# Optimization experiments

Measured on AMD Instinct MI355X. Metric: run time of the kernel, lower is better.

## Reference

```python
import jax, jax.numpy as jnp
import numpy as np


def setup_inputs() -> dict:
    key = jax.random.key(0)
    k1, k2 = jax.random.split(key)
    B, K = 128, 1024
    coordinates = jax.random.normal(k1, (B, K, 3), dtype=jnp.float32)
    precision_squared = jax.random.uniform(k2, (1,), dtype=jnp.float32)
    return {"coordinates": coordinates, "precision_squared": precision_squared}


def reference(coordinates, precision_squared):
    norms = jnp.sum(coordinates * coordinates, axis=-1)  # [B, K]
    gram = jnp.einsum('bkd,bjd->bkj', coordinates, coordinates)  # [B, K, K]
    distances = norms[:, :, None] - 2.0 * gram + norms[:, None, :]  # [B, K, K]
    A = jnp.exp(-distances * precision_squared[0])
    A = jax.nn.softmax(A, axis=-1)  # row softmax (axis=1 of the per-sample [K,K])
    return A
```

## Files before the change

kernel.cpp:

```cpp
#include <hip/hip_runtime.h>


#define K_PTS 1024
#define ROWS_PER_BLOCK 4

__global__ __launch_bounds__(256) void adj_softmax_kernel(
    const float* __restrict__ coords,
    const float* __restrict__ prec,
    float* __restrict__ out,
    int B) {
  __shared__ float sx[K_PTS];
  __shared__ float sy[K_PTS];
  __shared__ float sz[K_PTS];

  const int tid  = threadIdx.x;
  const int lane = tid & 63;
  const int wave = tid >> 6;
  const int tilesPerBatch = K_PTS / ROWS_PER_BLOCK;
  const int b    = blockIdx.x / tilesPerBatch;
  const int tile = blockIdx.x % tilesPerBatch;

  const float p = prec[0];

  {
    const float* cb = coords + (size_t)b * (K_PTS * 3);
    const int p0 = tid * 4;
    const float4* src = (const float4*)(cb + (size_t)p0 * 3);
    float4 a0 = src[0];
    float4 a1 = src[1];
    float4 a2 = src[2];
    sx[p0 + 0] = a0.x; sy[p0 + 0] = a0.y; sz[p0 + 0] = a0.z;
    sx[p0 + 1] = a0.w; sy[p0 + 1] = a1.x; sz[p0 + 1] = a1.y;
    sx[p0 + 2] = a1.z; sy[p0 + 2] = a1.w; sz[p0 + 2] = a2.x;
    sx[p0 + 3] = a2.y; sy[p0 + 3] = a2.z; sz[p0 + 3] = a2.w;
  }
  __syncthreads();

  const int i = tile * ROWS_PER_BLOCK + wave;
  const float xi = sx[i];
  const float yi = sy[i];
  const float zi = sz[i];

  float4 e[4];
  float acc = 0.0f;

#pragma unroll
  for (int t = 0; t < 4; ++t) {
    const int j0 = 4 * lane + 256 * t;
    float4 vx = *(const float4*)&sx[j0];
    float4 vy = *(const float4*)&sy[j0];
    float4 vz = *(const float4*)&sz[j0];

    float dx, dy, dz, d, xv;
    float4 ev;

    dx = vx.x - xi; dy = vy.x - yi; dz = vz.x - zi;
    d  = fmaf(dx, dx, fmaf(dy, dy, dz * dz));
    xv = __expf(-p * d);
    ev.x = __expf(xv - 1.0f);

    dx = vx.y - xi; dy = vy.y - yi; dz = vz.y - zi;
    d  = fmaf(dx, dx, fmaf(dy, dy, dz * dz));
    xv = __expf(-p * d);
    ev.y = __expf(xv - 1.0f);

    dx = vx.z - xi; dy = vy.z - yi; dz = vz.z - zi;
    d  = fmaf(dx, dx, fmaf(dy, dy, dz * dz));
    xv = __expf(-p * d);
    ev.z = __expf(xv - 1.0f);

    dx = vx.w - xi; dy = vy.w - yi; dz = vz.w - zi;
    d  = fmaf(dx, dx, fmaf(dy, dy, dz * dz));
    xv = __expf(-p * d);
    ev.w = __expf(xv - 1.0f);

    e[t] = ev;
    acc += (ev.x + ev.y) + (ev.z + ev.w);
  }

#pragma unroll
  for (int off = 32; off > 0; off >>= 1) {
    acc += __shfl_xor(acc, off, 64);
  }
  const float inv = 1.0f / acc;

  float* orow = out + ((size_t)b * K_PTS + i) * K_PTS;
#pragma unroll
  for (int t = 0; t < 4; ++t) {
    float4 ev = e[t];
    ev.x *= inv; ev.y *= inv; ev.z *= inv; ev.w *= inv;
    *(float4*)&orow[4 * lane + 256 * t] = ev;
  }
}

extern "C" void kernel_launch(void* const* d_in, const int* in_sizes, int n_in,
                              void* d_out, int out_size, void* d_ws, size_t ws_size,
                              hipStream_t stream) {
  const float* coords = (const float*)d_in[0];
  const float* prec   = (const float*)d_in[1];
  float* out = (float*)d_out;

  const int B = in_sizes[0] / (K_PTS * 3);
  const int grid = B * (K_PTS / ROWS_PER_BLOCK);

  adj_softmax_kernel<<<grid, 256, 0, stream>>>(coords, prec, out, B);
}
```

Baseline: 512.3 us.

## Process multiple row tiles per block and use nontemporal output stores

Each block now stages a batch's coordinates into shared memory once and loops over 64 rows instead of 4. Column coordinates are kept in registers across rows, which cuts redundant global loads, LDS staging and block launch overhead. Output stores become nontemporal to avoid cache pollution on the large write stream. Fewer blocks reduce parallel slack and raise register pressure.

```diff
diff --git a/kernel.cpp b/kernel.cpp
--- a/kernel.cpp
+++ b/kernel.cpp
@@ -2,9 +2,13 @@
 
 
 #define K_PTS 1024
-#define ROWS_PER_BLOCK 4
+#define THREADS 256
+#define TILES_PER_BLOCK 16
+#define BLOCKS_PER_BATCH 16
 
-__global__ __launch_bounds__(256) void adj_softmax_kernel(
+typedef float vf4 __attribute__((ext_vector_type(4)));
+
+__global__ __launch_bounds__(THREADS, 4) void adj_softmax_kernel(
     const float* __restrict__ coords,
     const float* __restrict__ prec,
     float* __restrict__ out,
@@ -13,14 +17,14 @@
   __shared__ float sy[K_PTS];
   __shared__ float sz[K_PTS];
 
-  const int tid  = threadIdx.x;
-  const int lane = tid & 63;
-  const int wave = tid >> 6;
-  const int tilesPerBatch = K_PTS / ROWS_PER_BLOCK;
-  const int b    = blockIdx.x / tilesPerBatch;
-  const int tile = blockIdx.x % tilesPerBatch;
+  const int tid   = threadIdx.x;
+  const int lane  = tid & 63;
+  const int wave  = tid >> 6;
+  const int b     = blockIdx.x / BLOCKS_PER_BATCH;
+  const int chunk = blockIdx.x % BLOCKS_PER_BATCH;
 
-  const float p = prec[0];
+  const float p  = prec[0];
+  const float np = -p;
 
   {
     const float* cb = coords + (size_t)b * (K_PTS * 3);
@@ -36,60 +40,67 @@
   }
   __syncthreads();
 
-  const int i = tile * ROWS_PER_BLOCK + wave;
-  const float xi = sx[i];
-  const float yi = sy[i];
-  const float zi = sz[i];
-
-  float4 e[4];
-  float acc = 0.0f;
-
+  float4 vx[4], vy[4], vz[4];
 #pragma unroll
   for (int t = 0; t < 4; ++t) {
     const int j0 = 4 * lane + 256 * t;
-    float4 vx = *(const float4*)&sx[j0];
-    float4 vy = *(const float4*)&sy[j0];
-    float4 vz = *(const float4*)&sz[j0];
-
-    float dx, dy, dz, d, xv;
-    float4 ev;
-
-    dx = vx.x - xi; dy = vy.x - yi; dz = vz.x - zi;
-    d  = fmaf(dx, dx, fmaf(dy, dy, dz * dz));
-    xv = __expf(-p * d);
-    ev.x = __expf(xv - 1.0f);
-
-    dx = vx.y - xi; dy = vy.y - yi; dz = vz.y - zi;
-    d  = fmaf(dx, dx, fmaf(dy, dy, dz * dz));
-    xv = __expf(-p * d);
-    ev.y = __expf(xv - 1.0f);
-
-    dx = vx.z - xi; dy = vy.z - yi; dz = vz.z - zi;
-    d  = fmaf(dx, dx, fmaf(dy, dy, dz * dz));
-    xv = __expf(-p * d);
-    ev.z = __expf(xv - 1.0f);
-
-    dx = vx.w - xi; dy = vy.w - yi; dz = vz.w - zi;
-    d  = fmaf(dx, dx, fmaf(dy, dy, dz * dz));
-    xv = __expf(-p * d);
-    ev.w = __expf(xv - 1.0f);
-
-    e[t] = ev;
-    acc += (ev.x + ev.y) + (ev.z + ev.w);
+    vx[t] = *(const float4*)&sx[j0];
+    vy[t] = *(const float4*)&sy[j0];
+    vz[t] = *(const float4*)&sz[j0];
   }
 
+  float* ob = out + (size_t)b * K_PTS * K_PTS;
+
+  for (int it = 0; it < TILES_PER_BLOCK; ++it) {
+    const int i = chunk * (TILES_PER_BLOCK * 4) + it * 4 + wave;
+    const float xi = sx[i];
+    const float yi = sy[i];
+    const float zi = sz[i];
+
+    vf4 e[4];
+    float acc = 0.0f;
+
 #pragma unroll
-  for (int off = 32; off > 0; off >>= 1) {
-    acc += __shfl_xor(acc, off, 64);
-  }
-  const float inv = 1.0f / acc;
+    for (int t = 0; t < 4; ++t) {
+      float dx, dy, dz, d, xv;
+      vf4 ev;
 
-  float* orow = out + ((size_t)b * K_PTS + i) * K_PTS;
+      dx = vx[t].x - xi; dy = vy[t].x - yi; dz = vz[t].x - zi;
+      d  = fmaf(dx, dx, fmaf(dy, dy, dz * dz));
+      xv = __expf(np * d);
+      ev.x = __expf(xv - 1.0f);
+
+      dx = vx[t].y - xi; dy = vy[t].y - yi; dz = vz[t].y - zi;
+      d  = fmaf(dx, dx, fmaf(dy, dy, dz * dz));
+      xv = __expf(np * d);
+      ev.y = __expf(xv - 1.0f);
+
+      dx = vx[t].z - xi; dy = vy[t].z - yi; dz = vz[t].z - zi;
+      d  = fmaf(dx, dx, fmaf(dy, dy, dz * dz));
+      xv = __expf(np * d);
+      ev.z = __expf(xv - 1.0f);
+
+      dx = vx[t].w - xi; dy = vy[t].w - yi; dz = vz[t].w - zi;
+      d  = fmaf(dx, dx, fmaf(dy, dy, dz * dz));
+      xv = __expf(np * d);
+      ev.w = __expf(xv - 1.0f);
+
+      e[t] = ev;
+      acc += (ev.x + ev.y) + (ev.z + ev.w);
+    }
+
 #pragma unroll
-  for (int t = 0; t < 4; ++t) {
-    float4 ev = e[t];
-    ev.x *= inv; ev.y *= inv; ev.z *= inv; ev.w *= inv;
-    *(float4*)&orow[4 * lane + 256 * t] = ev;
+    for (int off = 32; off > 0; off >>= 1) {
+      acc += __shfl_xor(acc, off, 64);
+    }
+    const float inv = 1.0f / acc;
+
+    float* orow = ob + (size_t)i * K_PTS;
+#pragma unroll
+    for (int t = 0; t < 4; ++t) {
+      vf4 ev = e[t] * inv;
+      __builtin_nontemporal_store(ev, (vf4*)&orow[4 * lane + 256 * t]);
+    }
   }
 }
 
@@ -101,7 +112,7 @@
   float* out = (float*)d_out;
 
   const int B = in_sizes[0] / (K_PTS * 3);
-  const int grid = B * (K_PTS / ROWS_PER_BLOCK);
+  const int grid = B * BLOCKS_PER_BATCH;
 
-  adj_softmax_kernel<<<grid, 256, 0, stream>>>(coords, prec, out, B);
+  adj_softmax_kernel<<<grid, THREADS, 0, stream>>>(coords, prec, out, B);
 }
```

Result: slower. 523.6 us (+2.2%).
